# Optimization experiments

Hardware: AMD Instinct MI355X
Metric: run time of the kernel (lower is better)

The kernel has to match this reference:

```python
import jax, jax.numpy as jnp
import numpy as np
import math

D = 1024
H = 1024
N = 32
T = 1024

def setup_inputs() -> dict:
    key = jax.random.key(0)
    k1, k2, k3, k4 = jax.random.split(key, 4)
    x = jax.random.normal(k1, (N, T, D), dtype=jnp.float32)
    h0 = jax.random.normal(k2, (N, H), dtype=jnp.float32)
    Wx = jax.random.normal(k3, (D, 4 * H), dtype=jnp.float32) / math.sqrt(D)
    Wh = jax.random.normal(k4, (H, 4 * H), dtype=jnp.float32) / math.sqrt(H)
    b = jnp.zeros((4 * H,), dtype=jnp.float32)
    return {"x": x, "h0": h0, "Wx": Wx, "Wh": Wh, "b": b}

def reference(x, h0, Wx, Wh, b):
    # Hoist input projection into one big GEMM: (N,T,D)@(D,4H) -> (N,T,4H)
    xW = jnp.einsum('ntd,dh->nth', x, Wx) + b  # (N, T, 4H)
    Hd = h0.shape[1]

    def step(carry, xw_t):
        prev_h, prev_c = carry
        a = xw_t + prev_h @ Wh  # (N, 4H)
        a_i, a_f, a_o, a_g = jnp.split(a, 4, axis=-1)
        i = jax.nn.sigmoid(a_i)
        f = jax.nn.sigmoid(a_f)
        o = jax.nn.sigmoid(a_o)
        g = jnp.tanh(a_g)
        next_c = f * prev_c + i * g
        next_h = o * jnp.tanh(next_c)
        return (next_h, next_c), next_h

    c0 = jnp.zeros_like(h0)
    xW_t = jnp.swapaxes(xW, 0, 1)  # (T, N, 4H)
    _, hs = jax.lax.scan(step, (h0, c0), xW_t)
    return jnp.swapaxes(hs, 0, 1)  # (N, T, H)
```

## Files before the change

kernel.cpp:

```cpp
#include <hip/hip_runtime.h>
#include <cstdio>
#include <cstdint>

#define TT 1024
#define DD 1024
#define HH 1024
#define NN 32
#define G4 4096

using bf16x8   = __attribute__((ext_vector_type(8))) __bf16;
using f32x4    = __attribute__((ext_vector_type(4))) float;
using uint32x4 = __attribute__((ext_vector_type(4))) unsigned int;

typedef const __attribute__((address_space(1))) void* gas_cp;
typedef __attribute__((address_space(3))) void* las_p;

__device__ __forceinline__ unsigned short f2bf(float f) {
  unsigned int u = __builtin_bit_cast(unsigned int, f);
  u = u + 0x7fffu + ((u >> 16) & 1u);
  return (unsigned short)(u >> 16);
}
__device__ __forceinline__ float bf2f(unsigned short s) {
  unsigned int u = ((unsigned int)s) << 16;
  return __builtin_bit_cast(float, u);
}
__device__ __forceinline__ float sigm(float x) { return 1.f / (1.f + __expf(-x)); }
__device__ __forceinline__ float tanh_f(float x) {
  float a = fabsf(x);
  float e = __expf(-2.f * a);
  float r = (1.f - e) / (1.f + e);
  return x < 0.f ? -r : r;
}

__global__ void cast_bf4(const float4* __restrict__ in, uint2* __restrict__ o, int n4) {
  int i = blockIdx.x * 256 + threadIdx.x;
  if (i < n4) {
    float4 v = in[i];
    uint2 r;
    r.x = (unsigned int)f2bf(v.x) | ((unsigned int)f2bf(v.y) << 16);
    r.y = (unsigned int)f2bf(v.z) | ((unsigned int)f2bf(v.w) << 16);
    o[i] = r;
  }
}

__global__ void transp_cast(const float* __restrict__ in, unsigned short* __restrict__ outT,
                            int R, int C) {
  __shared__ unsigned short t[64][65];
  int nbc = C >> 6;
  int tc = blockIdx.x % nbc, tr = blockIdx.x / nbc;
  int r0 = tr << 6, c0 = tc << 6;
  for (int i = threadIdx.x; i < 4096; i += 256) {
    int r = i >> 6, c = i & 63;
    t[c][r] = f2bf(in[(size_t)(r0 + r) * C + c0 + c]);
  }
  __syncthreads();
  for (int i = threadIdx.x; i < 4096; i += 256) {
    int c = i >> 6, r = i & 63;
    outT[(size_t)(c0 + c) * R + r0 + r] = t[c][r];
  }
}

__global__ void pack_h0(const float* __restrict__ in, unsigned int* __restrict__ o) {
  int i = blockIdx.x * 256 + threadIdx.x;
  o[i] = (unsigned int)f2bf(in[i]);
}

#define BM 128
#define BN 128
#define BK 64

__launch_bounds__(256, 2)
__global__ void gemm_xw(const unsigned short* __restrict__ A,
                        const unsigned short* __restrict__ B,
                        const float* __restrict__ bias,
                        unsigned short* __restrict__ C)
{
  __shared__ alignas(16) unsigned short As[BM * BK];
  __shared__ alignas(16) unsigned short Bs[BN * BK];
  int bid = blockIdx.x;
  int swz = (bid & 7) * 1024 + (bid >> 3);
  int grp = swz >> 8;
  int loc = swz & 255;
  int tm = (grp << 3) + (loc & 7);
  int tn = loc >> 3;
  int tid = threadIdx.x;
  int w = tid >> 6, lane = tid & 63;
  int wr = w >> 1, wc = w & 1;

  f32x4 acc[4][4] = {};

  const size_t rowA0 = (size_t)tm * BM;
  const size_t colB0 = (size_t)tn * BN;

  for (int k0 = 0; k0 < DD; k0 += BK) {
    #pragma unroll
    for (int i = 0; i < 4; ++i) {
      int chunk = w * 4 + i;
      int p = chunk * 1024 + lane * 16;
      int row = p >> 7;
      int bo = p & 127;
      int gb = bo ^ ((row & 7) << 4);
      const char* ga = (const char*)(A + (rowA0 + row) * DD + k0) + gb;
      __builtin_amdgcn_global_load_lds((gas_cp)ga, (las_p)((char*)As + chunk * 1024), 16, 0, 0);
      const char* gB = (const char*)(B + (colB0 + row) * DD + k0) + gb;
      __builtin_amdgcn_global_load_lds((gas_cp)gB, (las_p)((char*)Bs + chunk * 1024), 16, 0, 0);
    }
    __syncthreads();

    #pragma unroll
    for (int ks = 0; ks < 2; ++ks) {
      bf16x8 af[4], bfr[4];
      #pragma unroll
      for (int mi = 0; mi < 4; ++mi) {
        int row = wr * 64 + mi * 16 + (lane & 15);
        int kb = (ks * 32 + ((lane >> 4) << 3)) * 2;
        af[mi] = *(const bf16x8*)((const char*)As + row * 128 + (kb ^ ((row & 7) << 4)));
      }
      #pragma unroll
      for (int ni = 0; ni < 4; ++ni) {
        int row = wc * 64 + ni * 16 + (lane & 15);
        int kb = (ks * 32 + ((lane >> 4) << 3)) * 2;
        bfr[ni] = *(const bf16x8*)((const char*)Bs + row * 128 + (kb ^ ((row & 7) << 4)));
      }
      #pragma unroll
      for (int mi = 0; mi < 4; ++mi)
        #pragma unroll
        for (int ni = 0; ni < 4; ++ni)
          acc[mi][ni] = __builtin_amdgcn_mfma_f32_16x16x32_bf16(af[mi], bfr[ni], acc[mi][ni], 0, 0, 0);
    }
    __syncthreads();
  }

  #pragma unroll
  for (int ni = 0; ni < 4; ++ni) {
    int col = (int)colB0 + wc * 64 + ni * 16 + (lane & 15);
    float bb = bias[col];
    int g = col >> 10, J = col & 1023;
    int jw2 = J >> 5, jc2 = J & 31;
    #pragma unroll
    for (int mi = 0; mi < 4; ++mi) {
      #pragma unroll
      for (int r = 0; r < 4; ++r) {
        size_t row = rowA0 + wr * 64 + mi * 16 + ((lane >> 4) << 2) + r;
        size_t n2 = row >> 10, t2 = row & 1023;
        size_t cl = n2 >> 2, rr = n2 & 3;
        C[((((t2 * 8 + cl) * 32 + jw2) * 4 + rr) * 32 + jc2) * 4 + g] = f2bf(acc[mi][ni][r] + bb);
      }
    }
  }
}

#define LDA0(dst, ptr, off) asm volatile("global_load_dwordx2 %0, %1, off offset:" #off " sc0" : "=v"(dst) : "v"(ptr))
#define LDA1(dst, ptr, off) asm volatile("global_load_dwordx2 %0, %1, off offset:" #off " sc0 sc1" : "=v"(dst) : "v"(ptr))
#define LDW(dst, addr, off) asm volatile("global_load_dwordx4 %0, %1, off offset:" #off : "=v"(dst) : "v"(addr))

#define POLLCHUNK(r0, r1, r2, r3, o0, o1, o2, o3)                              \
  { int rc_ = 0;                                                               \
    for (;;) {                                                                 \
      if (!(rc_ & 1)) { LDA0(r0,hq,o0); LDA0(r1,hq,o1); LDA0(r2,hq,o2); LDA0(r3,hq,o3); } \
      else            { LDA1(r0,hq,o0); LDA1(r1,hq,o1); LDA1(r2,hq,o2); LDA1(r3,hq,o3); } \
      asm volatile("s_waitcnt vmcnt(0)");                                      \
      __builtin_amdgcn_sched_barrier(0);                                       \
      unsigned long long bad_ = ((r0 & M64) ^ pat) | ((r1 & M64) ^ pat) |      \
                                ((r2 & M64) ^ pat) | ((r3 & M64) ^ pat);       \
      if (!__any(bad_ != 0)) break;                                            \
      __builtin_amdgcn_s_sleep(1);                                             \
      ++rc_;                                                                   \
    } }

#define RESOLVECHUNK(r0, r1, r2, r3, o0, o1, o2, o3)                           \
  { asm volatile("s_waitcnt vmcnt(0)");                                        \
    __builtin_amdgcn_sched_barrier(0);                                         \
    unsigned long long bad_ = ((r0 & M64) ^ pat) | ((r1 & M64) ^ pat) |        \
                              ((r2 & M64) ^ pat) | ((r3 & M64) ^ pat);         \
    if (__any(bad_ != 0)) {                                                    \
      __builtin_amdgcn_s_sleep(1);                                             \
      POLLCHUNK(r0, r1, r2, r3, o0, o1, o2, o3)                                \
    } }

#define PREFCHUNK(r0, r1, r2, r3, o0, o1, o2, o3)                              \
  { LDA0(r0,hq,o0); LDA0(r1,hq,o1); LDA0(r2,hq,o2); LDA0(r3,hq,o3); }

__launch_bounds__(512, 1)
__global__ void lstm_rec(const unsigned long long* __restrict__ xw,
                         const unsigned short* __restrict__ WhT,
                         unsigned int* __restrict__ hbuf,
                         float* __restrict__ out)
{
  __shared__ float red[2][8][4][128];

  const int bid = blockIdx.x;
  const int cl = bid & 7;
  const int jw = bid >> 3;
  const int j0 = jw * 32;
  const int tid = threadIdx.x;
  const int lane = tid & 63;
  const int kq = tid >> 6;
  const int l15 = lane & 15;
  const int q4 = lane >> 4;

  bf16x8 Bf[8][4];
  #pragma unroll
  for (int tile = 0; tile < 8; ++tile) {
    int cc = tile * 16 + l15;
    int gcol = (cc >> 5) * 1024 + j0 + (cc & 31);
    const unsigned short* wb = WhT + (size_t)gcol * HH + kq * 128 + q4 * 8;
    LDW(Bf[tile][0], wb, 0);
    LDW(Bf[tile][1], wb, 64);
    LDW(Bf[tile][2], wb, 128);
    LDW(Bf[tile][3], wb, 192);
  }
  asm volatile("s_waitcnt vmcnt(0)");

  const bool ld = (l15 < 4);
  const int r4row = lane & 3;
  const bool ep = (lane < 16);
  const int ecell = kq * 16 + l15;
  const int er = ecell >> 5, ej = ecell & 31;
  float c = 0.f;
  const unsigned long long M64 = 0xFFFF0000FFFF0000ULL;

  unsigned long long u0=0,u1=0,u2=0,u3=0,u4=0,u5=0,u6=0,u7=0,
                     u8=0,u9=0,u10=0,u11=0,u12=0,u13=0,u14=0,u15=0;

  unsigned long long xq = 0;
  if (ep) xq = xw[(((size_t)0 * 8 + cl) * 32 + jw) * 128 + ecell];

  #pragma unroll 1
  for (int t = 0; t < TT; ++t) {
    const int par = t & 1;
    const unsigned int* hc = hbuf + (size_t)par * 32768 + cl * 4096;
    unsigned int* hn = hbuf + (size_t)(par ^ 1) * 32768 + cl * 4096;

    const unsigned long long pat =
        ((unsigned long long)(unsigned)t << 16) | ((unsigned long long)(unsigned)t << 48);
    const unsigned long long* hq =
        (const unsigned long long*)(hc + (size_t)r4row * 1024 + kq * 128 + q4 * 8);

    f32x4 acc[8] = {};
    {
      uint32x4 wv;
      #define KSTEP(ks, a0, a1, a2, a3)                                              \
        wv[0] = __builtin_amdgcn_perm((unsigned)((a0) >> 32), (unsigned)(a0), 0x05040100u); \
        wv[1] = __builtin_amdgcn_perm((unsigned)((a1) >> 32), (unsigned)(a1), 0x05040100u); \
        wv[2] = __builtin_amdgcn_perm((unsigned)((a2) >> 32), (unsigned)(a2), 0x05040100u); \
        wv[3] = __builtin_amdgcn_perm((unsigned)((a3) >> 32), (unsigned)(a3), 0x05040100u); \
        { bf16x8 av = __builtin_bit_cast(bf16x8, wv);                                \
          _Pragma("unroll")                                                          \
          for (int tile = 0; tile < 8; ++tile)                                       \
            acc[tile] = __builtin_amdgcn_mfma_f32_16x16x32_bf16(av, Bf[tile][ks], acc[tile], 0, 0, 0); }

      if (ld) {
        POLLCHUNK(u0, u1, u2, u3, 0, 8, 16, 24)
        PREFCHUNK(u4, u5, u6, u7, 128, 136, 144, 152)
      }
      KSTEP(0, u0, u1, u2, u3)

      if (ld) {
        RESOLVECHUNK(u4, u5, u6, u7, 128, 136, 144, 152)
        PREFCHUNK(u8, u9, u10, u11, 256, 264, 272, 280)
      }
      KSTEP(1, u4, u5, u6, u7)

      if (ld) {
        RESOLVECHUNK(u8, u9, u10, u11, 256, 264, 272, 280)
        PREFCHUNK(u12, u13, u14, u15, 384, 392, 400, 408)
      }
      KSTEP(2, u8, u9, u10, u11)

      if (ld) {
        RESOLVECHUNK(u12, u13, u14, u15, 384, 392, 400, 408)
      }
      KSTEP(3, u12, u13, u14, u15)
      #undef KSTEP
    }

    unsigned long long xq_n = 0;
    if (ep) {
      int tp = (t + 1 < TT) ? t + 1 : 0;
      xq_n = xw[(((size_t)tp * 8 + cl) * 32 + jw) * 128 + ecell];
    }

    if (q4 == 0) {
      #pragma unroll
      for (int tile = 0; tile < 8; ++tile)
        #pragma unroll
        for (int rg = 0; rg < 4; ++rg)
          red[par][kq][rg][tile * 16 + l15] = acc[tile][rg];
    }
    __syncthreads();

    if (ep) {
      float s0 = 0.f, s1 = 0.f, s2 = 0.f, s3 = 0.f;
      #pragma unroll
      for (int k2 = 0; k2 < 8; ++k2) {
        s0 += red[par][k2][er][ej];
        s1 += red[par][k2][er][32 + ej];
        s2 += red[par][k2][er][64 + ej];
        s3 += red[par][k2][er][96 + ej];
      }
      float ai  = s0 + bf2f((unsigned short)xq);
      float af_ = s1 + bf2f((unsigned short)(xq >> 16));
      float ao  = s2 + bf2f((unsigned short)(xq >> 32));
      float ag  = s3 + bf2f((unsigned short)(xq >> 48));
      float ig = sigm(ai), fg = sigm(af_), og = sigm(ao);
      float gg = tanh_f(ag);
      c = fg * c + ig * gg;
      float hv = og * tanh_f(c);

      unsigned int hp = (unsigned int)f2bf(hv) | ((unsigned int)(t + 1) << 16);
      __hip_atomic_store(hn + (size_t)er * 1024 + j0 + ej, hp,
                         __ATOMIC_RELAXED, __HIP_MEMORY_SCOPE_AGENT);
      out[((size_t)(cl * 4 + er) * TT + t) * HH + j0 + ej] = hv;
    }
    xq = xq_n;
  }
}

extern "C" void kernel_launch(void* const* d_in, const int* in_sizes, int n_in,
                              void* d_out, int out_size, void* d_ws, size_t ws_size,
                              hipStream_t stream) {
  (void)in_sizes; (void)n_in; (void)out_size;
  const float* x  = (const float*)d_in[0];
  const float* h0 = (const float*)d_in[1];
  const float* Wx = (const float*)d_in[2];
  const float* Wh = (const float*)d_in[3];
  const float* b  = (const float*)d_in[4];
  float* out = (float*)d_out;

  char* ws = (char*)d_ws;
  size_t o_xw  = 0;
  size_t o_xbf = o_xw  + (size_t)32768 * 4096 * 2;
  size_t o_wxT = o_xbf + (size_t)32768 * 1024 * 2;
  size_t o_whT = o_wxT + (size_t)4096 * 1024 * 2;
  size_t o_hb  = o_whT + (size_t)4096 * 1024 * 2;
  size_t need  = o_hb  + (size_t)2 * 32768 * 4;
  if (ws_size < need) {
    fprintf(stderr, "kernel_launch: ws_size %zu < needed %zu\n", ws_size, need);
    return;
  }
  unsigned short* xw  = (unsigned short*)(ws + o_xw);
  unsigned short* xbf = (unsigned short*)(ws + o_xbf);
  unsigned short* wxT = (unsigned short*)(ws + o_wxT);
  unsigned short* whT = (unsigned short*)(ws + o_whT);
  unsigned int*   hb  = (unsigned int*)(ws + o_hb);

  hipMemsetAsync(hb, 0xFF, (size_t)2 * 32768 * 4, stream);
  pack_h0<<<128, 256, 0, stream>>>(h0, hb);
  cast_bf4<<<32768, 256, 0, stream>>>((const float4*)x, (uint2*)xbf, 33554432 / 4);
  transp_cast<<<1024, 256, 0, stream>>>(Wx, wxT, 1024, 4096);
  transp_cast<<<1024, 256, 0, stream>>>(Wh, whT, 1024, 4096);
  gemm_xw<<<8192, 256, 0, stream>>>(xbf, wxT, b, xw);

  void* args[] = { (void*)&xw, (void*)&whT, (void*)&hb, (void*)&out };
  hipLaunchCooperativeKernel(lstm_rec, dim3(256), dim3(512), args, 0, stream);
}
```

Measured before the change: 4.019 ms.

## Split each LSTM timestep into two batch-row passes to overlap polling and epilogue

```diff
diff --git a/kernel.cpp b/kernel.cpp
--- a/kernel.cpp
+++ b/kernel.cpp
@@ -181,6 +181,78 @@
 #define PREFCHUNK(r0, r1, r2, r3, o0, o1, o2, o3)                              \
   { LDA0(r0,hq,o0); LDA0(r1,hq,o1); LDA0(r2,hq,o2); LDA0(r3,hq,o3); }
 
+#define KSTEP(ks, a0, a1, a2, a3)                                              \
+  { uint32x4 wv;                                                               \
+    wv[0] = __builtin_amdgcn_perm((unsigned)((a0) >> 32), (unsigned)(a0), 0x05040100u); \
+    wv[1] = __builtin_amdgcn_perm((unsigned)((a1) >> 32), (unsigned)(a1), 0x05040100u); \
+    wv[2] = __builtin_amdgcn_perm((unsigned)((a2) >> 32), (unsigned)(a2), 0x05040100u); \
+    wv[3] = __builtin_amdgcn_perm((unsigned)((a3) >> 32), (unsigned)(a3), 0x05040100u); \
+    bf16x8 av = __builtin_bit_cast(bf16x8, wv);                                \
+    _Pragma("unroll")                                                          \
+    for (int tile = 0; tile < 8; ++tile)                                       \
+      acc[tile] = __builtin_amdgcn_mfma_f32_16x16x32_bf16(av, Bf[tile][ks], acc[tile], 0, 0, 0); }
+
+#define PASS(G, tv, cvar, xqvar, xqnvar)                                       \
+  {                                                                            \
+    const int hpar = (tv) & 1;                                                 \
+    const unsigned int* hc = hbuf + (size_t)hpar * 32768 + cl * 4096;          \
+    unsigned int* hn = hbuf + (size_t)(hpar ^ 1) * 32768 + cl * 4096;          \
+    const unsigned long long pat =                                             \
+        ((unsigned long long)(unsigned)(tv) << 16) |                           \
+        ((unsigned long long)(unsigned)(tv) << 48);                            \
+    const unsigned long long* hq =                                             \
+        (const unsigned long long*)(hc + (size_t)r4row * 1024 + kq * 128 + q4 * 8); \
+    const bool myld = ((l15 >> 1) == (G));                                     \
+    f32x4 acc[8] = {};                                                         \
+    if (myld) { POLLCHUNK(u0, u1, u2, u3, 0, 8, 16, 24)                        \
+                PREFCHUNK(u4, u5, u6, u7, 128, 136, 144, 152) }                \
+    KSTEP(0, u0, u1, u2, u3)                                                   \
+    if (myld) { RESOLVECHUNK(u4, u5, u6, u7, 128, 136, 144, 152)               \
+                PREFCHUNK(u8, u9, u10, u11, 256, 264, 272, 280) }              \
+    KSTEP(1, u4, u5, u6, u7)                                                   \
+    if (myld) { RESOLVECHUNK(u8, u9, u10, u11, 256, 264, 272, 280)             \
+                PREFCHUNK(u12, u13, u14, u15, 384, 392, 400, 408) }            \
+    KSTEP(2, u8, u9, u10, u11)                                                 \
+    if (myld) { RESOLVECHUNK(u12, u13, u14, u15, 384, 392, 400, 408) }         \
+    KSTEP(3, u12, u13, u14, u15)                                               \
+    if (q4 == 0) {                                                             \
+      _Pragma("unroll")                                                        \
+      for (int tile = 0; tile < 8; ++tile)                                     \
+        _Pragma("unroll")                                                      \
+        for (int rg = 0; rg < 4; ++rg)                                         \
+          red[G][kq][rg][tile * 16 + l15] = acc[tile][rg];                     \
+    }                                                                          \
+    __syncthreads();                                                           \
+    if (epl) {                                                                 \
+      int tp = ((tv) + 1 < TT) ? (tv) + 1 : 0;                                 \
+      xqnvar = xw[(((size_t)tp * 8 + cl) * 32 + jw) * 128 + (G) * 64 + ecellg];\
+    }                                                                          \
+    if (epl) {                                                                 \
+      const int er_ = (G) * 2 + erg;                                           \
+      float s0 = 0.f, s1 = 0.f, s2 = 0.f, s3 = 0.f;                            \
+      _Pragma("unroll")                                                        \
+      for (int k2 = 0; k2 < 8; ++k2) {                                         \
+        s0 += red[G][k2][er_][ej];                                             \
+        s1 += red[G][k2][er_][32 + ej];                                        \
+        s2 += red[G][k2][er_][64 + ej];                                        \
+        s3 += red[G][k2][er_][96 + ej];                                        \
+      }                                                                        \
+      float ai  = s0 + bf2f((unsigned short)xqvar);                            \
+      float af_ = s1 + bf2f((unsigned short)(xqvar >> 16));                    \
+      float ao  = s2 + bf2f((unsigned short)(xqvar >> 32));                    \
+      float ag  = s3 + bf2f((unsigned short)(xqvar >> 48));                    \
+      float ig = sigm(ai), fg = sigm(af_), og = sigm(ao);                      \
+      float gg = tanh_f(ag);                                                   \
+      cvar = fg * cvar + ig * gg;                                              \
+      float hv = og * tanh_f(cvar);                                            \
+      unsigned int hp = (unsigned int)f2bf(hv) | ((unsigned int)((tv) + 1) << 16); \
+      __hip_atomic_store(hn + (size_t)er_ * 1024 + j0 + ej, hp,                \
+                         __ATOMIC_RELAXED, __HIP_MEMORY_SCOPE_AGENT);          \
+      out[((size_t)(cl * 4 + er_) * TT + (tv)) * HH + j0 + ej] = hv;           \
+    }                                                                          \
+    xqvar = xqnvar;                                                            \
+  }
+
 __launch_bounds__(512, 1)
 __global__ void lstm_rec(const unsigned long long* __restrict__ xw,
                          const unsigned short* __restrict__ WhT,
@@ -212,108 +284,27 @@
   }
   asm volatile("s_waitcnt vmcnt(0)");
 
-  const bool ld = (l15 < 4);
   const int r4row = lane & 3;
-  const bool ep = (lane < 16);
-  const int ecell = kq * 16 + l15;
-  const int er = ecell >> 5, ej = ecell & 31;
-  float c = 0.f;
+  const bool epl = (lane < 8);
+  const int ecellg = kq * 8 + lane;
+  const int erg = ecellg >> 5;
+  const int ej  = ecellg & 31;
+  float cA = 0.f, cB = 0.f;
   const unsigned long long M64 = 0xFFFF0000FFFF0000ULL;
 
   unsigned long long u0=0,u1=0,u2=0,u3=0,u4=0,u5=0,u6=0,u7=0,
                      u8=0,u9=0,u10=0,u11=0,u12=0,u13=0,u14=0,u15=0;
 
-  unsigned long long xq = 0;
-  if (ep) xq = xw[(((size_t)0 * 8 + cl) * 32 + jw) * 128 + ecell];
+  unsigned long long xqA = 0, xqB = 0, xqnA = 0, xqnB = 0;
+  if (epl) {
+    xqA = xw[(((size_t)0 * 8 + cl) * 32 + jw) * 128 + ecellg];
+    xqB = xw[(((size_t)0 * 8 + cl) * 32 + jw) * 128 + 64 + ecellg];
+  }
 
   #pragma unroll 1
   for (int t = 0; t < TT; ++t) {
-    const int par = t & 1;
-    const unsigned int* hc = hbuf + (size_t)par * 32768 + cl * 4096;
-    unsigned int* hn = hbuf + (size_t)(par ^ 1) * 32768 + cl * 4096;
-
-    const unsigned long long pat =
-        ((unsigned long long)(unsigned)t << 16) | ((unsigned long long)(unsigned)t << 48);
-    const unsigned long long* hq =
-        (const unsigned long long*)(hc + (size_t)r4row * 1024 + kq * 128 + q4 * 8);
-
-    f32x4 acc[8] = {};
-    {
-      uint32x4 wv;
-      #define KSTEP(ks, a0, a1, a2, a3)                                              \
-        wv[0] = __builtin_amdgcn_perm((unsigned)((a0) >> 32), (unsigned)(a0), 0x05040100u); \
-        wv[1] = __builtin_amdgcn_perm((unsigned)((a1) >> 32), (unsigned)(a1), 0x05040100u); \
-        wv[2] = __builtin_amdgcn_perm((unsigned)((a2) >> 32), (unsigned)(a2), 0x05040100u); \
-        wv[3] = __builtin_amdgcn_perm((unsigned)((a3) >> 32), (unsigned)(a3), 0x05040100u); \
-        { bf16x8 av = __builtin_bit_cast(bf16x8, wv);                                \
-          _Pragma("unroll")                                                          \
-          for (int tile = 0; tile < 8; ++tile)                                       \
-            acc[tile] = __builtin_amdgcn_mfma_f32_16x16x32_bf16(av, Bf[tile][ks], acc[tile], 0, 0, 0); }
-
-      if (ld) {
-        POLLCHUNK(u0, u1, u2, u3, 0, 8, 16, 24)
-        PREFCHUNK(u4, u5, u6, u7, 128, 136, 144, 152)
-      }
-      KSTEP(0, u0, u1, u2, u3)
-
-      if (ld) {
-        RESOLVECHUNK(u4, u5, u6, u7, 128, 136, 144, 152)
-        PREFCHUNK(u8, u9, u10, u11, 256, 264, 272, 280)
-      }
-      KSTEP(1, u4, u5, u6, u7)
-
-      if (ld) {
-        RESOLVECHUNK(u8, u9, u10, u11, 256, 264, 272, 280)
-        PREFCHUNK(u12, u13, u14, u15, 384, 392, 400, 408)
-      }
-      KSTEP(2, u8, u9, u10, u11)
-
-      if (ld) {
-        RESOLVECHUNK(u12, u13, u14, u15, 384, 392, 400, 408)
-      }
-      KSTEP(3, u12, u13, u14, u15)
-      #undef KSTEP
-    }
-
-    unsigned long long xq_n = 0;
-    if (ep) {
-      int tp = (t + 1 < TT) ? t + 1 : 0;
-      xq_n = xw[(((size_t)tp * 8 + cl) * 32 + jw) * 128 + ecell];
-    }
-
-    if (q4 == 0) {
-      #pragma unroll
-      for (int tile = 0; tile < 8; ++tile)
-        #pragma unroll
-        for (int rg = 0; rg < 4; ++rg)
-          red[par][kq][rg][tile * 16 + l15] = acc[tile][rg];
-    }
-    __syncthreads();
-
-    if (ep) {
-      float s0 = 0.f, s1 = 0.f, s2 = 0.f, s3 = 0.f;
-      #pragma unroll
-      for (int k2 = 0; k2 < 8; ++k2) {
-        s0 += red[par][k2][er][ej];
-        s1 += red[par][k2][er][32 + ej];
-        s2 += red[par][k2][er][64 + ej];
-        s3 += red[par][k2][er][96 + ej];
-      }
-      float ai  = s0 + bf2f((unsigned short)xq);
-      float af_ = s1 + bf2f((unsigned short)(xq >> 16));
-      float ao  = s2 + bf2f((unsigned short)(xq >> 32));
-      float ag  = s3 + bf2f((unsigned short)(xq >> 48));
-      float ig = sigm(ai), fg = sigm(af_), og = sigm(ao);
-      float gg = tanh_f(ag);
-      c = fg * c + ig * gg;
-      float hv = og * tanh_f(c);
-
-      unsigned int hp = (unsigned int)f2bf(hv) | ((unsigned int)(t + 1) << 16);
-      __hip_atomic_store(hn + (size_t)er * 1024 + j0 + ej, hp,
-                         __ATOMIC_RELAXED, __HIP_MEMORY_SCOPE_AGENT);
-      out[((size_t)(cl * 4 + er) * TT + t) * HH + j0 + ej] = hv;
-    }
-    xq = xq_n;
+    PASS(0, t, cA, xqA, xqnA)
+    PASS(1, t, cB, xqB, xqnB)
   }
 }
 
```

Result: slower. 5.617 ms (+39.8%).
